# Optimization experiments

Hardware: AMD Instinct MI355X
Metric: run time of the kernel (lower is better)

## Reference

```python
import jax, jax.numpy as jnp
from jax import lax
import numpy as np

N, B, P, D, DOUT, MAXDEG = 81920, 4096, 20, 128, 256, 8
EPS = 1e-5

def _bn(x, g, b):
    m = x.mean(0)
    v = x.var(0)
    return (x - m) / jnp.sqrt(v + EPS) * g + b

def setup_inputs() -> dict:
    key = jax.random.key(0)
    ks = jax.random.split(key, 24)
    s = 0.05
    return {
        'feat': jax.random.normal(ks[0], (N, D), jnp.float32),
        'intend': jax.random.normal(ks[1], (B, D), jnp.float32),
        'position_weight': jax.random.uniform(ks[2], (N,), jnp.float32),
        'nbr_idx': jax.random.randint(ks[3], (N, MAXDEG), 0, N),
        'deg': jax.random.randint(ks[4], (N,), 0, MAXDEG + 1),
        'last_nodes': jax.random.randint(ks[5], (B,), 0, N),
        # EOPA params
        'bn1_g': jnp.ones((D,), jnp.float32),
        'bn1_b': jnp.zeros((D,), jnp.float32),
        'W_ih': jax.random.normal(ks[6], (3 * D, D), jnp.float32) * s,
        'W_hh': jax.random.normal(ks[7], (3 * D, D), jnp.float32) * s,
        'b_ih': jax.random.normal(ks[8], (3 * D,), jnp.float32) * s,
        'b_hh': jax.random.normal(ks[9], (3 * D,), jnp.float32) * s,
        'W_self': jax.random.normal(ks[10], (D, D), jnp.float32) * s,
        'W_neigh': jax.random.normal(ks[11], (D, D), jnp.float32) * s,
        # AttnReadout params (hidden_dim == D)
        'bn2_g': jnp.ones((D,), jnp.float32),
        'bn2_b': jnp.zeros((D,), jnp.float32),
        'Wu': jax.random.normal(ks[12], (D, D), jnp.float32) * s,
        'Wv': jax.random.normal(ks[13], (D, D), jnp.float32) * s,
        'bv': jax.random.normal(ks[14], (D,), jnp.float32) * s,
        'Wi': jax.random.normal(ks[15], (D, D), jnp.float32) * s,
        'bi': jax.random.normal(ks[16], (D,), jnp.float32) * s,
        'We': jax.random.normal(ks[17], (D, 1), jnp.float32) * s,
        'Wout': jax.random.normal(ks[18], (DOUT, D), jnp.float32) * s,
    }

def reference(feat, intend, position_weight, nbr_idx, deg, last_nodes,
              bn1_g, bn1_b, W_ih, W_hh, b_ih, b_hh, W_self, W_neigh,
              bn2_g, bn2_b, Wu, Wv, bv, Wi, bi, We, Wout):
    # ---- EOPA: gather mailbox -> GRU over neighbors -> self + neigh mix ----
    h0 = _bn(feat, bn1_g, bn1_b)              # BatchNorm1d (batch stats)
    mail = h0[nbr_idx]                        # [N, MAXDEG, D] gather
    xs = jnp.moveaxis(mail, 0, 1)             # [MAXDEG, N, D]

    def gru_step(h, tx):
        t, x = tx
        gi = x @ W_ih.T + b_ih                # [N, 3D]
        gh = h @ W_hh.T + b_hh
        ir, iz, inn = jnp.split(gi, 3, axis=1)
        hr, hz, hn = jnp.split(gh, 3, axis=1)
        r = jax.nn.sigmoid(ir + hr)
        z = jax.nn.sigmoid(iz + hz)
        n = jnp.tanh(inn + r * hn)
        h_new = (1.0 - z) * n + z * h
        # freeze state past each node's true mailbox length (ragged GRU)
        h = jnp.where((t < deg)[:, None], h_new, h)
        return h, None

    neigh, _ = lax.scan(gru_step, jnp.zeros((N, D), feat.dtype),
                        (jnp.arange(MAXDEG), xs))
    rst = h0 @ W_self.T + neigh @ W_neigh.T   # [N, D], activation=None

    # ---- AttnReadout: segment softmax attention + segment sums ----
    h = _bn(rst, bn2_g, bn2_b)
    fu = (h @ Wu.T).reshape(B, P, D)
    fv = (intend @ Wv.T + bv)[:, None, :]         # broadcast_nodes
    fl = (h[last_nodes] @ Wi.T + bi)[:, None, :]  # broadcast_nodes
    e = (jax.nn.sigmoid(fu + fv + fl) @ We)[..., 0]   # [B, P]
    alpha = jax.nn.softmax(e, axis=1)[..., None]      # segment_softmax
    hg = h.reshape(B, P, D)
    rst_g = (hg * alpha).sum(axis=1) @ Wout.T         # segment_sum + fc_out
    pos = (hg * position_weight.reshape(B, P, 1)).sum(axis=1) @ Wout.T
    return rst_g, pos
```

## Files before the change

kernel.cpp:

```cpp
#include <hip/hip_runtime.h>

#define NN      81920
#define BB      4096
#define PP      20
#define DD      128
#define DOUTT   256
#define MAXDEGG 8
#define NBLK_B  160

using bf16x8 = __attribute__((ext_vector_type(8))) short;
using f32x4  = __attribute__((ext_vector_type(4))) float;
using u16x4  = __attribute__((ext_vector_type(4))) ushort;

__device__ __forceinline__ float b2f(ushort u) {
    union { unsigned u; float f; } v; v.u = ((unsigned)u) << 16; return v.f;
}
__device__ __forceinline__ ushort f2b(float f) {
    union { float f; unsigned u; } v; v.f = f;
    unsigned r = v.u + 0x7fffu + ((v.u >> 16) & 1u);
    return (ushort)(r >> 16);
}
__device__ __forceinline__ float sigm(float x) {
    return __fdividef(1.f, 1.f + __expf(-x));
}
__device__ __forceinline__ float tanh_fast(float x) {
    return 1.f - __fdividef(2.f, 1.f + __expf(2.f * x));
}
__device__ __forceinline__ f32x4 mfma16(bf16x8 a, bf16x8 b, f32x4 c) {
    return __builtin_amdgcn_mfma_f32_16x16x32_bf16(a, b, c, 0, 0, 0);
}
__device__ __forceinline__ bf16x8 pack8(float4 a, float4 b) {
    bf16x8 r;
    r[0] = (short)f2b(a.x); r[1] = (short)f2b(a.y);
    r[2] = (short)f2b(a.z); r[3] = (short)f2b(a.w);
    r[4] = (short)f2b(b.x); r[5] = (short)f2b(b.y);
    r[6] = (short)f2b(b.z); r[7] = (short)f2b(b.w);
    return r;
}
__device__ __forceinline__ bf16x8 ld8_bf(const ushort* p) { return *(const bf16x8*)p; }
__device__ __forceinline__ bf16x8 ld8_f32(const float* p) {
    return pack8(*(const float4*)p, *(const float4*)(p + 4));
}

__global__ __launch_bounds__(512) void hist_k(const int* __restrict__ deg,
                                              int* __restrict__ blockHist) {
    __shared__ int wh[8][9];
    const int t = threadIdx.x, w = t >> 6, lane = t & 63;
    int d = deg[blockIdx.x * 512 + t]; d = min(max(d, 0), 8);
#pragma unroll
    for (int c = 0; c < 9; ++c) {
        unsigned long long m = __ballot(d == c);
        if (lane == 0) wh[w][c] = __popcll(m);
    }
    __syncthreads();
    if (t < 9) {
        int s = 0;
#pragma unroll
        for (int w2 = 0; w2 < 8; ++w2) s += wh[w2][t];
        blockHist[blockIdx.x * 9 + t] = s;
    }
}
__global__ void scan_k(const int* __restrict__ blockHist,
                       int* __restrict__ blockBase) {
    __shared__ int classTot[9], classStart[9];
    const int c = threadIdx.x;
    if (c < 9) {
        int s = 0;
        for (int b = 0; b < NBLK_B; ++b) s += blockHist[b * 9 + c];
        classTot[c] = s;
    }
    __syncthreads();
    if (c == 0) {
        int acc = 0;
        for (int k = 0; k < 9; ++k) { classStart[k] = acc; acc += classTot[k]; }
    }
    __syncthreads();
    if (c < 9) {
        int acc = classStart[c];
        for (int b = 0; b < NBLK_B; ++b) {
            blockBase[b * 9 + c] = acc;
            acc += blockHist[b * 9 + c];
        }
    }
}
__global__ __launch_bounds__(512) void scatter_k(const int* __restrict__ deg,
                                                 const int* __restrict__ blockBase,
                                                 int* __restrict__ perm) {
    __shared__ int wh[8][9];
    __shared__ int wbase[8][9];
    const int t = threadIdx.x, w = t >> 6, lane = t & 63;
    const int i = blockIdx.x * 512 + t;
    int d = deg[i]; d = min(max(d, 0), 8);
    int lt = 0;
#pragma unroll
    for (int c = 0; c < 9; ++c) {
        unsigned long long m = __ballot(d == c);
        if (lane == 0) wh[w][c] = __popcll(m);
        if (d == c) lt = __popcll(m & ((1ull << lane) - 1ull));
    }
    __syncthreads();
    if (t < 72) {
        const int w2 = t / 9, c = t - w2 * 9;
        int s = blockBase[blockIdx.x * 9 + c];
        for (int k = 0; k < w2; ++k) s += wh[k][c];
        wbase[w2][c] = s;
    }
    __syncthreads();
    perm[wbase[w][d] + lt] = i;
}

__global__ __launch_bounds__(256) void bn_stats(const float* __restrict__ X,
                                                float* __restrict__ part) {
    const int tid  = threadIdx.x;
    const int col  = tid & 127;
    const int half = tid >> 7;
    const long base = (long)blockIdx.x * 128 + (long)half * 64;
    float s = 0.f, q = 0.f;
    for (int i = 0; i < 64; ++i) {
        float x = X[(base + i) * 128 + col];
        s += x; q += x * x;
    }
    __shared__ float red[2][2][128];
    red[0][half][col] = s;
    red[1][half][col] = q;
    __syncthreads();
    if (tid < 128) {
        part[blockIdx.x * 128 + tid]             = red[0][0][tid] + red[0][1][tid];
        part[640 * 128 + blockIdx.x * 128 + tid] = red[1][0][tid] + red[1][1][tid];
    }
}

__global__ __launch_bounds__(256) void bn_final(const float* __restrict__ part, int nparts,
                                                const float* __restrict__ g,
                                                const float* __restrict__ b,
                                                float2* __restrict__ ss) {
    const int c = blockIdx.x;
    const int t = threadIdx.x;
    float s = 0.f, q = 0.f;
    for (int i = t; i < nparts; i += 256) {
        s += part[(long)i * 128 + c];
        q += part[(long)(nparts + i) * 128 + c];
    }
#pragma unroll
    for (int off = 32; off > 0; off >>= 1) {
        s += __shfl_xor(s, off, 64);
        q += __shfl_xor(q, off, 64);
    }
    __shared__ float rs[4], rq[4];
    if ((t & 63) == 0) { rs[t >> 6] = s; rq[t >> 6] = q; }
    __syncthreads();
    if (t == 0) {
        s = rs[0] + rs[1] + rs[2] + rs[3];
        q = rq[0] + rq[1] + rq[2] + rq[3];
        const float inv_n = 1.f / (float)NN;
        float mean = s * inv_n;
        float var  = q * inv_n - mean * mean;
        float rstd = rsqrtf(var + 1e-5f);
        float sc = g[c] * rstd;
        ss[c] = make_float2(sc, b[c] - mean * sc);
    }
}

template <int NCOL, int KPARTS, bool A1F32, bool GATHER2, bool BIAS1, bool BIAS2,
          bool FOLD1, bool FOLD2, int OUTMODE>
__global__ __launch_bounds__(256) void gemm_bt(
    const void* __restrict__ A1, const void* __restrict__ A2,
    const float* __restrict__ W1, const float* __restrict__ W2,
    const float* __restrict__ bias1, const float* __restrict__ bias2,
    const float2* __restrict__ ssW1, const float2* __restrict__ ssW2,
    const int* __restrict__ gidx, void* __restrict__ outv,
    float* __restrict__ part, int nparts,
    const float* __restrict__ fvl, const float* __restrict__ We,
    float* __restrict__ e) {
    constexpr int JT = NCOL / 64;
    __shared__ float epart[4][64];
    const int tid = threadIdx.x;
    const int w   = tid >> 6;
    const int l   = tid & 63;
    const int l15 = l & 15;
    const int l4  = l >> 4;
    const int colbase = w * (NCOL / 4);

    bf16x8 bfr[JT][KPARTS * 4];
    float bv[JT];
    float Wec[JT];
#pragma unroll
    for (int jl = 0; jl < JT; ++jl) {
        const int wrow = colbase + jl * 16 + l15;
        float fb = 0.f;
#pragma unroll
        for (int kp = 0; kp < KPARTS; ++kp) {
            const float* Wp = (kp == 0) ? W1 : W2;
            const float2* sp = (kp == 0) ? ssW1 : ssW2;
            const bool fold = (kp == 0) ? FOLD1 : FOLD2;
#pragma unroll
            for (int kt = 0; kt < 4; ++kt) {
                const float* wp = &Wp[(long)wrow * 128 + kt * 32 + l4 * 8];
                float4 a = *(const float4*)wp;
                float4 b4 = *(const float4*)(wp + 4);
                if (fold) {
                    const float* s = (const float*)(sp + kt * 32 + l4 * 8);
                    float4 s0 = *(const float4*)s, s1 = *(const float4*)(s + 4);
                    float4 s2 = *(const float4*)(s + 8), s3 = *(const float4*)(s + 12);
                    fb += s0.y * a.x + s0.w * a.y + s1.y * a.z + s1.w * a.w
                        + s2.y * b4.x + s2.w * b4.y + s3.y * b4.z + s3.w * b4.w;
                    a.x *= s0.x; a.y *= s0.z; a.z *= s1.x; a.w *= s1.z;
                    b4.x *= s2.x; b4.y *= s2.z; b4.z *= s3.x; b4.w *= s3.z;
                }
                bfr[jl][kp * 4 + kt] = pack8(a, b4);
            }
        }
        if (FOLD1 || FOLD2) {
            fb += __shfl_xor(fb, 16, 64);
            fb += __shfl_xor(fb, 32, 64);
        }
        if (BIAS1) fb += bias1[wrow];
        if (BIAS2) fb += bias2[wrow];
        bv[jl] = fb;
        if (OUTMODE == 3) Wec[jl] = We[wrow];
    }

    const int rowblk = blockIdx.x * 64;
    const f32x4 fz = {0.f, 0.f, 0.f, 0.f};
    float ssum[JT], sq[JT];
#pragma unroll
    for (int jl = 0; jl < JT; ++jl) { ssum[jl] = 0.f; sq[jl] = 0.f; }

#pragma unroll
    for (int it = 0; it < 4; ++it) {
        const int arow1 = rowblk + it * 16 + l15;
        bf16x8 afr[KPARTS * 4];
#pragma unroll
        for (int kt = 0; kt < 4; ++kt) {
            if (A1F32)
                afr[kt] = ld8_f32(&((const float*)A1)[(long)arow1 * 128 + kt * 32 + l4 * 8]);
            else
                afr[kt] = ld8_bf(&((const ushort*)A1)[(long)arow1 * 128 + kt * 32 + l4 * 8]);
        }
        if (KPARTS == 2) {
            const long arow2 = GATHER2 ? (long)gidx[arow1] : (long)arow1;
#pragma unroll
            for (int kt = 0; kt < 4; ++kt)
                afr[4 + kt] = ld8_bf(&((const ushort*)A2)[arow2 * 128 + kt * 32 + l4 * 8]);
        }
        f32x4 acc[JT];
#pragma unroll
        for (int jl = 0; jl < JT; ++jl) {
            acc[jl] = fz;
#pragma unroll
            for (int kk = 0; kk < KPARTS * 4; ++kk)
                acc[jl] = mfma16(afr[kk], bfr[jl][kk], acc[jl]);
        }
        float ps[4] = {0.f, 0.f, 0.f, 0.f};
#pragma unroll
        for (int jl = 0; jl < JT; ++jl) {
            const int col = colbase + jl * 16 + l15;
#pragma unroll
            for (int r = 0; r < 4; ++r) {
                const long orow = rowblk + it * 16 + l4 * 4 + r;
                float v = acc[jl][r] + bv[jl];
                if (OUTMODE == 0 || OUTMODE == 2)
                    ((ushort*)outv)[orow * NCOL + col] = f2b(v);
                if (OUTMODE == 1)
                    ((float*)outv)[orow * NCOL + col] = v;
                if (OUTMODE == 2) { ssum[jl] += v; sq[jl] += v * v; }
                if (OUTMODE == 3) {
                    const int b = (int)orow / PP;
                    ps[r] += sigm(v + fvl[(long)b * 128 + col]) * Wec[jl];
                }
            }
        }
        if (OUTMODE == 3) {
#pragma unroll
            for (int r = 0; r < 4; ++r) {
#pragma unroll
                for (int off = 1; off < 16; off <<= 1)
                    ps[r] += __shfl_xor(ps[r], off, 64);
            }
            if (l15 == 0) {
#pragma unroll
                for (int r = 0; r < 4; ++r)
                    epart[w][it * 16 + l4 * 4 + r] = ps[r];
            }
        }
    }
    if (OUTMODE == 2) {
#pragma unroll
        for (int jl = 0; jl < JT; ++jl) {
            float s = ssum[jl], q = sq[jl];
            s += __shfl_xor(s, 16, 64); s += __shfl_xor(s, 32, 64);
            q += __shfl_xor(q, 16, 64); q += __shfl_xor(q, 32, 64);
            if (l4 == 0) {
                const int col = colbase + jl * 16 + l15;
                part[(long)blockIdx.x * 128 + col] = s;
                part[(long)nparts * 128 + (long)blockIdx.x * 128 + col] = q;
            }
        }
    }
    if (OUTMODE == 3) {
        __syncthreads();
        if (tid < 64)
            e[rowblk + tid] = epart[0][tid] + epart[1][tid] + epart[2][tid] + epart[3][tid];
    }
}

__global__ __attribute__((amdgpu_flat_work_group_size(512, 512), amdgpu_waves_per_eu(4, 4)))
void gru_kernel(const ushort* __restrict__ G,
                const float* __restrict__ Whh,
                const float* __restrict__ bhh,
                const int* __restrict__ nbr_idx,
                const int* __restrict__ deg,
                const int* __restrict__ perm,
                ushort* __restrict__ neigh) {
    __shared__ alignas(16) ushort hbuf[2][64][136];
    __shared__ alignas(16) int nbrs[64][8];
    __shared__ int degs[64];
    __shared__ int nid[64];

    const int tid = threadIdx.x;
    const int w   = tid >> 6;
    const int l   = tid & 63;
    const int l15 = l & 15;
    const int l4  = l >> 4;
    const int blockRow = (gridDim.x - 1 - blockIdx.x) * 64;
    const int colbase = w * 16;
    const int c0 = colbase + l4 * 4;

    if (tid < 64) nid[tid] = perm[blockRow + tid];
    {
        bf16x8 z = {0, 0, 0, 0, 0, 0, 0, 0};
        bf16x8* p = (bf16x8*)&hbuf[0][0][0];
        for (int i = tid; i < 64 * 136 / 8; i += 512) p[i] = z;
    }
    __syncthreads();
    nbrs[tid >> 3][tid & 7] = nbr_idx[(long)nid[tid >> 3] * 8 + (tid & 7)];
    if (tid < 64) degs[tid] = deg[nid[tid]];

    bf16x8 bfr[3][4];
#pragma unroll
    for (int g = 0; g < 3; ++g)
#pragma unroll
        for (int kt = 0; kt < 4; ++kt)
            bfr[g][kt] = ld8_f32(&Whh[(long)(g * 128 + colbase + l15) * 128 + kt * 32 + l4 * 8]);
    f32x4 binit[3];
#pragma unroll
    for (int g = 0; g < 3; ++g)
        binit[g] = *(const f32x4*)&bhh[g * 128 + c0];
    __syncthreads();

    int dreg[4];
#pragma unroll
    for (int it = 0; it < 4; ++it) dreg[it] = degs[it * 16 + l15];
    int dmax = degs[l];
#pragma unroll
    for (int off = 32; off > 0; off >>= 1) dmax = max(dmax, __shfl_xor(dmax, off, 64));
    dmax = __builtin_amdgcn_readfirstlane(dmax);

    u16x4 gP[2][3];
#pragma unroll
    for (int it = 0; it < 2; ++it) {
        gP[it][0] = (u16x4){0,0,0,0}; gP[it][1] = (u16x4){0,0,0,0}; gP[it][2] = (u16x4){0,0,0,0};
        if (0 < dreg[it]) {
            const ushort* Grow = G + (long)nbrs[it * 16 + l15][0] * 384;
            gP[it][0] = *(const u16x4*)&Grow[c0];
            gP[it][1] = *(const u16x4*)&Grow[c0 + 128];
            gP[it][2] = *(const u16x4*)&Grow[c0 + 256];
        }
    }

    int cur = 0;
    for (int t = 0; t < dmax; ++t) {
        u16x4 g23[2][3];
#pragma unroll
        for (int it = 2; it < 4; ++it) {
            u16x4* gd = g23[it - 2];
            gd[0] = (u16x4){0,0,0,0}; gd[1] = (u16x4){0,0,0,0}; gd[2] = (u16x4){0,0,0,0};
            if (t < dreg[it]) {
                const ushort* Grow = G + (long)nbrs[it * 16 + l15][t] * 384;
                gd[0] = *(const u16x4*)&Grow[c0];
                gd[1] = *(const u16x4*)&Grow[c0 + 128];
                gd[2] = *(const u16x4*)&Grow[c0 + 256];
            }
        }

#pragma unroll
        for (int it = 0; it < 2; ++it) {
            const int row = it * 16 + l15;
            const bool upd = (t < dreg[it]);
            bf16x8 af[4];
#pragma unroll
            for (int kt = 0; kt < 4; ++kt)
                af[kt] = *(const bf16x8*)&hbuf[cur][row][kt * 32 + l4 * 8];
            f32x4 ar = binit[0], az = binit[1], an = binit[2];
#pragma unroll
            for (int kt = 0; kt < 4; ++kt) {
                ar = mfma16(bfr[0][kt], af[kt], ar);
                az = mfma16(bfr[1][kt], af[kt], az);
                an = mfma16(bfr[2][kt], af[kt], an);
            }
            const u16x4 hold = *(const u16x4*)&hbuf[cur][row][c0];
            u16x4 hnew = hold;
            if (upd) {
#pragma unroll
                for (int r = 0; r < 4; ++r) {
                    const float rr = sigm(b2f(gP[it][0][r]) + ar[r]);
                    const float zz = sigm(b2f(gP[it][1][r]) + az[r]);
                    const float nn = tanh_fast(b2f(gP[it][2][r]) + rr * an[r]);
                    hnew[r] = f2b((1.f - zz) * nn + zz * b2f(hold[r]));
                }
            }
            *(u16x4*)&hbuf[1 - cur][row][c0] = hnew;
        }

#pragma unroll
        for (int it = 0; it < 2; ++it) {
            gP[it][0] = (u16x4){0,0,0,0}; gP[it][1] = (u16x4){0,0,0,0}; gP[it][2] = (u16x4){0,0,0,0};
            if (t + 1 < dreg[it]) {
                const ushort* Grow = G + (long)nbrs[it * 16 + l15][t + 1] * 384;
                gP[it][0] = *(const u16x4*)&Grow[c0];
                gP[it][1] = *(const u16x4*)&Grow[c0 + 128];
                gP[it][2] = *(const u16x4*)&Grow[c0 + 256];
            }
        }

#pragma unroll
        for (int it = 2; it < 4; ++it) {
            const int row = it * 16 + l15;
            const bool upd = (t < dreg[it]);
            bf16x8 af[4];
#pragma unroll
            for (int kt = 0; kt < 4; ++kt)
                af[kt] = *(const bf16x8*)&hbuf[cur][row][kt * 32 + l4 * 8];
            f32x4 ar = binit[0], az = binit[1], an = binit[2];
#pragma unroll
            for (int kt = 0; kt < 4; ++kt) {
                ar = mfma16(bfr[0][kt], af[kt], ar);
                az = mfma16(bfr[1][kt], af[kt], az);
                an = mfma16(bfr[2][kt], af[kt], an);
            }
            const u16x4 hold = *(const u16x4*)&hbuf[cur][row][c0];
            u16x4 hnew = hold;
            if (upd) {
#pragma unroll
                for (int r = 0; r < 4; ++r) {
                    const float rr = sigm(b2f(g23[it - 2][0][r]) + ar[r]);
                    const float zz = sigm(b2f(g23[it - 2][1][r]) + az[r]);
                    const float nn = tanh_fast(b2f(g23[it - 2][2][r]) + rr * an[r]);
                    hnew[r] = f2b((1.f - zz) * nn + zz * b2f(hold[r]));
                }
            }
            *(u16x4*)&hbuf[1 - cur][row][c0] = hnew;
        }
        __syncthreads();
        cur ^= 1;
    }
    for (int idx = tid; idx < 64 * 16; idx += 512) {
        const int row = idx >> 4, ch = idx & 15;
        bf16x8* dst = (bf16x8*)(neigh + (long)nid[row] * 128);
        dst[ch] = *(const bf16x8*)&hbuf[cur][row][ch * 8];
    }
}

__global__ __launch_bounds__(256) void seg_k(const ushort* __restrict__ rst,
                                             const float* __restrict__ e,
                                             const float* __restrict__ pw,
                                             const float2* __restrict__ ss2,
                                             ushort* __restrict__ s12) {
    const int g = blockIdx.x * 2 + (threadIdx.x >> 7);
    const int c = threadIdx.x & 127;
    const float2 sc = ss2[c];
    float ev[PP];
    float m = -1e30f;
#pragma unroll
    for (int p = 0; p < PP; ++p) { ev[p] = e[g * PP + p]; m = fmaxf(m, ev[p]); }
    float sum = 0.f;
#pragma unroll
    for (int p = 0; p < PP; ++p) { ev[p] = __expf(ev[p] - m); sum += ev[p]; }
    const float inv = __fdividef(1.f, sum);
    float a1 = 0.f, a2 = 0.f;
#pragma unroll
    for (int p = 0; p < PP; ++p) {
        const int node = g * PP + p;
        const float hv = b2f(rst[(long)node * 128 + c]) * sc.x + sc.y;
        a1 += (ev[p] * inv) * hv;
        a2 += pw[node] * hv;
    }
    s12[(long)g * 128 + c]        = f2b(a1);
    s12[(long)(BB + g) * 128 + c] = f2b(a2);
}

extern "C" void kernel_launch(void* const* d_in, const int* in_sizes, int n_in,
                              void* d_out, int out_size, void* d_ws, size_t ws_size,
                              hipStream_t stream) {
    const float* feat    = (const float*)d_in[0];
    const float* intend  = (const float*)d_in[1];
    const float* pw      = (const float*)d_in[2];
    const int*   nbr_idx = (const int*)d_in[3];
    const int*   deg     = (const int*)d_in[4];
    const int*   last    = (const int*)d_in[5];
    const float* bn1_g   = (const float*)d_in[6];
    const float* bn1_b   = (const float*)d_in[7];
    const float* W_ih    = (const float*)d_in[8];
    const float* W_hh    = (const float*)d_in[9];
    const float* b_ih    = (const float*)d_in[10];
    const float* b_hh    = (const float*)d_in[11];
    const float* W_self  = (const float*)d_in[12];
    const float* W_neigh = (const float*)d_in[13];
    const float* bn2_g   = (const float*)d_in[14];
    const float* bn2_b   = (const float*)d_in[15];
    const float* Wu      = (const float*)d_in[16];
    const float* Wv      = (const float*)d_in[17];
    const float* bv      = (const float*)d_in[18];
    const float* Wi      = (const float*)d_in[19];
    const float* bi      = (const float*)d_in[20];
    const float* We      = (const float*)d_in[21];
    const float* Wout    = (const float*)d_in[22];
    float* out = (float*)d_out;
    char* ws = (char*)d_ws;

    ushort* G     = (ushort*)(ws + 0L);
    ushort* rst   = G;
    ushort* neigh = (ushort*)(ws + 62914560L);
    float*  fvl   = (float*)(ws + 83886080L);
    float*  e     = (float*)(ws + 85983232L);
    ushort* s12   = (ushort*)(ws + 86310912L);
    float*  part1 = (float*)(ws + 88408064L);
    float*  part2 = (float*)(ws + 89063424L);
    int*    perm  = (int*)(ws + 90374144L);
    float2* ss1   = (float2*)(ws + 90701824L);
    float2* ss2   = (float2*)(ws + 90702848L);
    int*    blockHist = (int*)(ws + 90703872L);
    int*    blockBase = (int*)(ws + 90709632L);

    bn_stats<<<640, 256, 0, stream>>>(feat, part1);
    bn_final<<<128, 256, 0, stream>>>(part1, 640, bn1_g, bn1_b, ss1);

    hist_k<<<NBLK_B, 512, 0, stream>>>(deg, blockHist);
    scan_k<<<1, 16, 0, stream>>>(blockHist, blockBase);
    scatter_k<<<NBLK_B, 512, 0, stream>>>(deg, blockBase, perm);

    gemm_bt<384, 1, true, false, true, false, true, false, 0><<<1280, 256, 0, stream>>>(
        feat, nullptr, W_ih, nullptr, b_ih, nullptr, ss1, nullptr,
        nullptr, G, nullptr, 0, nullptr, nullptr, nullptr);

    gru_kernel<<<1280, 512, 0, stream>>>(G, W_hh, b_hh, nbr_idx, deg, perm, neigh);

    gemm_bt<128, 2, true, false, false, false, true, false, 2><<<1280, 256, 0, stream>>>(
        feat, neigh, W_self, W_neigh, nullptr, nullptr, ss1, nullptr,
        nullptr, rst, part2, 1280, nullptr, nullptr, nullptr);
    bn_final<<<128, 256, 0, stream>>>(part2, 1280, bn2_g, bn2_b, ss2);

    gemm_bt<128, 2, true, true, true, true, false, true, 1><<<64, 256, 0, stream>>>(
        intend, rst, Wv, Wi, bv, bi, nullptr, ss2,
        last, fvl, nullptr, 0, nullptr, nullptr, nullptr);

    gemm_bt<128, 1, false, false, false, false, true, false, 3><<<1280, 256, 0, stream>>>(
        rst, nullptr, Wu, nullptr, nullptr, nullptr, ss2, nullptr,
        nullptr, nullptr, nullptr, 0, fvl, We, e);

    seg_k<<<2048, 256, 0, stream>>>(rst, e, pw, ss2, s12);

    gemm_bt<256, 1, false, false, false, false, false, false, 1><<<128, 256, 0, stream>>>(
        s12, nullptr, Wout, nullptr, nullptr, nullptr, nullptr, nullptr,
        nullptr, out, nullptr, 0, nullptr, nullptr, nullptr);

    (void)in_sizes; (void)n_in; (void)out_size; (void)ws_size;
}
```

Before: 328.7 us.

## Fuse BN stats with degree histogram, fold GRU biases, widen GEMM blocks

Merges the BN-stats and degree-histogram kernels into one launch, and the BN-final and scan kernels into another, which cuts the launch count. Folds the r/z parts of b_hh into the input-projection GEMM bias so the GRU only adds the n-gate hidden bias. Doubles GEMM workgroups to 512 threads with fewer columns per wave. Restructures the GRU loop with macros and unconditional clamped gathers, so zero-degree rows now issue loads they do not need.

New measurement: 398.3 us. 21.2% more time.

```diff
diff --git a/kernel.cpp b/kernel.cpp
--- a/kernel.cpp
+++ b/kernel.cpp
@@ -6,7 +6,7 @@
 #define DD      128
 #define DOUTT   256
 #define MAXDEGG 8
-#define NBLK_B  160
+#define NBLK_H  320
 
 using bf16x8 = __attribute__((ext_vector_type(8))) short;
 using f32x4  = __attribute__((ext_vector_type(4))) float;
@@ -42,54 +42,110 @@
     return pack8(*(const float4*)p, *(const float4*)(p + 4));
 }
 
-__global__ __launch_bounds__(512) void hist_k(const int* __restrict__ deg,
-                                              int* __restrict__ blockHist) {
-    __shared__ int wh[8][9];
-    const int t = threadIdx.x, w = t >> 6, lane = t & 63;
-    int d = deg[blockIdx.x * 512 + t]; d = min(max(d, 0), 8);
-#pragma unroll
-    for (int c = 0; c < 9; ++c) {
-        unsigned long long m = __ballot(d == c);
-        if (lane == 0) wh[w][c] = __popcll(m);
-    }
-    __syncthreads();
-    if (t < 9) {
-        int s = 0;
-#pragma unroll
-        for (int w2 = 0; w2 < 8; ++w2) s += wh[w2][t];
-        blockHist[blockIdx.x * 9 + t] = s;
-    }
-}
-__global__ void scan_k(const int* __restrict__ blockHist,
-                       int* __restrict__ blockBase) {
-    __shared__ int classTot[9], classStart[9];
-    const int c = threadIdx.x;
-    if (c < 9) {
-        int s = 0;
-        for (int b = 0; b < NBLK_B; ++b) s += blockHist[b * 9 + c];
-        classTot[c] = s;
-    }
-    __syncthreads();
-    if (c == 0) {
-        int acc = 0;
-        for (int k = 0; k < 9; ++k) { classStart[k] = acc; acc += classTot[k]; }
-    }
-    __syncthreads();
-    if (c < 9) {
-        int acc = classStart[c];
-        for (int b = 0; b < NBLK_B; ++b) {
-            blockBase[b * 9 + c] = acc;
-            acc += blockHist[b * 9 + c];
-        }
-    }
-}
-__global__ __launch_bounds__(512) void scatter_k(const int* __restrict__ deg,
+__global__ __launch_bounds__(256) void stats_hist_k(const float* __restrict__ X,
+                                                    const int* __restrict__ deg,
+                                                    float* __restrict__ part,
+                                                    int* __restrict__ blockHist) {
+    const int tid = threadIdx.x;
+    if (blockIdx.x < 640) {
+        const int col  = tid & 127;
+        const int half = tid >> 7;
+        const long base = (long)blockIdx.x * 128 + (long)half * 64;
+        float s = 0.f, q = 0.f;
+        for (int i = 0; i < 64; ++i) {
+            float x = X[(base + i) * 128 + col];
+            s += x; q += x * x;
+        }
+        __shared__ float red[2][2][128];
+        red[0][half][col] = s;
+        red[1][half][col] = q;
+        __syncthreads();
+        if (tid < 128) {
+            part[blockIdx.x * 128 + tid]             = red[0][0][tid] + red[0][1][tid];
+            part[640 * 128 + blockIdx.x * 128 + tid] = red[1][0][tid] + red[1][1][tid];
+        }
+    } else {
+        __shared__ int wh[4][9];
+        const int hb = blockIdx.x - 640;
+        const int w = tid >> 6, lane = tid & 63;
+        int d = deg[hb * 256 + tid]; d = min(max(d, 0), 8);
+#pragma unroll
+        for (int c = 0; c < 9; ++c) {
+            unsigned long long m = __ballot(d == c);
+            if (lane == 0) wh[w][c] = __popcll(m);
+        }
+        __syncthreads();
+        if (tid < 9) {
+            int s = 0;
+#pragma unroll
+            for (int w2 = 0; w2 < 4; ++w2) s += wh[w2][tid];
+            blockHist[hb * 9 + tid] = s;
+        }
+    }
+}
+
+__global__ __launch_bounds__(256) void bnfinal_scan_k(const float* __restrict__ part, int nparts,
+                                                      const float* __restrict__ g,
+                                                      const float* __restrict__ b,
+                                                      float2* __restrict__ ss,
+                                                      const int* __restrict__ blockHist,
+                                                      int* __restrict__ blockBase) {
+    const int t = threadIdx.x;
+    if (blockIdx.x < 128) {
+        const int c = blockIdx.x;
+        float s = 0.f, q = 0.f;
+        for (int i = t; i < nparts; i += 256) {
+            s += part[(long)i * 128 + c];
+            q += part[(long)(nparts + i) * 128 + c];
+        }
+#pragma unroll
+        for (int off = 32; off > 0; off >>= 1) {
+            s += __shfl_xor(s, off, 64);
+            q += __shfl_xor(q, off, 64);
+        }
+        __shared__ float rs[4], rq[4];
+        if ((t & 63) == 0) { rs[t >> 6] = s; rq[t >> 6] = q; }
+        __syncthreads();
+        if (t == 0) {
+            s = rs[0] + rs[1] + rs[2] + rs[3];
+            q = rq[0] + rq[1] + rq[2] + rq[3];
+            const float inv_n = 1.f / (float)NN;
+            float mean = s * inv_n;
+            float var  = q * inv_n - mean * mean;
+            float rstd = rsqrtf(var + 1e-5f);
+            float sc = g[c] * rstd;
+            ss[c] = make_float2(sc, b[c] - mean * sc);
+        }
+    } else {
+        __shared__ int classTot[9], classStart[9];
+        if (t < 9) {
+            int s = 0;
+            for (int b2 = 0; b2 < NBLK_H; ++b2) s += blockHist[b2 * 9 + t];
+            classTot[t] = s;
+        }
+        __syncthreads();
+        if (t == 0) {
+            int acc = 0;
+            for (int k = 0; k < 9; ++k) { classStart[k] = acc; acc += classTot[k]; }
+        }
+        __syncthreads();
+        if (t < 9) {
+            int acc = classStart[t];
+            for (int b2 = 0; b2 < NBLK_H; ++b2) {
+                blockBase[b2 * 9 + t] = acc;
+                acc += blockHist[b2 * 9 + t];
+            }
+        }
+    }
+}
+
+__global__ __launch_bounds__(256) void scatter_k(const int* __restrict__ deg,
                                                  const int* __restrict__ blockBase,
                                                  int* __restrict__ perm) {
-    __shared__ int wh[8][9];
-    __shared__ int wbase[8][9];
+    __shared__ int wh[4][9];
+    __shared__ int wbase[4][9];
     const int t = threadIdx.x, w = t >> 6, lane = t & 63;
-    const int i = blockIdx.x * 512 + t;
+    const int i = blockIdx.x * 256 + t;
     int d = deg[i]; d = min(max(d, 0), 8);
     int lt = 0;
 #pragma unroll
@@ -99,7 +155,7 @@
         if (d == c) lt = __popcll(m & ((1ull << lane) - 1ull));
     }
     __syncthreads();
-    if (t < 72) {
+    if (t < 36) {
         const int w2 = t / 9, c = t - w2 * 9;
         int s = blockBase[blockIdx.x * 9 + c];
         for (int k = 0; k < w2; ++k) s += wh[k][c];
@@ -109,77 +165,25 @@
     perm[wbase[w][d] + lt] = i;
 }
 
-__global__ __launch_bounds__(256) void bn_stats(const float* __restrict__ X,
-                                                float* __restrict__ part) {
-    const int tid  = threadIdx.x;
-    const int col  = tid & 127;
-    const int half = tid >> 7;
-    const long base = (long)blockIdx.x * 128 + (long)half * 64;
-    float s = 0.f, q = 0.f;
-    for (int i = 0; i < 64; ++i) {
-        float x = X[(base + i) * 128 + col];
-        s += x; q += x * x;
-    }
-    __shared__ float red[2][2][128];
-    red[0][half][col] = s;
-    red[1][half][col] = q;
-    __syncthreads();
-    if (tid < 128) {
-        part[blockIdx.x * 128 + tid]             = red[0][0][tid] + red[0][1][tid];
-        part[640 * 128 + blockIdx.x * 128 + tid] = red[1][0][tid] + red[1][1][tid];
-    }
-}
-
-__global__ __launch_bounds__(256) void bn_final(const float* __restrict__ part, int nparts,
-                                                const float* __restrict__ g,
-                                                const float* __restrict__ b,
-                                                float2* __restrict__ ss) {
-    const int c = blockIdx.x;
-    const int t = threadIdx.x;
-    float s = 0.f, q = 0.f;
-    for (int i = t; i < nparts; i += 256) {
-        s += part[(long)i * 128 + c];
-        q += part[(long)(nparts + i) * 128 + c];
-    }
-#pragma unroll
-    for (int off = 32; off > 0; off >>= 1) {
-        s += __shfl_xor(s, off, 64);
-        q += __shfl_xor(q, off, 64);
-    }
-    __shared__ float rs[4], rq[4];
-    if ((t & 63) == 0) { rs[t >> 6] = s; rq[t >> 6] = q; }
-    __syncthreads();
-    if (t == 0) {
-        s = rs[0] + rs[1] + rs[2] + rs[3];
-        q = rq[0] + rq[1] + rq[2] + rq[3];
-        const float inv_n = 1.f / (float)NN;
-        float mean = s * inv_n;
-        float var  = q * inv_n - mean * mean;
-        float rstd = rsqrtf(var + 1e-5f);
-        float sc = g[c] * rstd;
-        ss[c] = make_float2(sc, b[c] - mean * sc);
-    }
-}
-
 template <int NCOL, int KPARTS, bool A1F32, bool GATHER2, bool BIAS1, bool BIAS2,
           bool FOLD1, bool FOLD2, int OUTMODE>
-__global__ __launch_bounds__(256) void gemm_bt(
+__global__ __launch_bounds__(512) void gemm_bt(
     const void* __restrict__ A1, const void* __restrict__ A2,
     const float* __restrict__ W1, const float* __restrict__ W2,
-    const float* __restrict__ bias1, const float* __restrict__ bias2,
+    const float* __restrict__ bias1, const float* __restrict__ bias2, int blim,
     const float2* __restrict__ ssW1, const float2* __restrict__ ssW2,
     const int* __restrict__ gidx, void* __restrict__ outv,
     float* __restrict__ part, int nparts,
     const float* __restrict__ fvl, const float* __restrict__ We,
     float* __restrict__ e) {
-    constexpr int JT = NCOL / 64;
-    __shared__ float epart[4][64];
+    constexpr int JT = NCOL / 128;
+    __shared__ float epart[8][64];
     const int tid = threadIdx.x;
     const int w   = tid >> 6;
     const int l   = tid & 63;
     const int l15 = l & 15;
     const int l4  = l >> 4;
-    const int colbase = w * (NCOL / 4);
+    const int colbase = w * (NCOL / 8);
 
     bf16x8 bfr[JT][KPARTS * 4];
     float bv[JT];
@@ -215,7 +219,7 @@
             fb += __shfl_xor(fb, 32, 64);
         }
         if (BIAS1) fb += bias1[wrow];
-        if (BIAS2) fb += bias2[wrow];
+        if (BIAS2) fb += (wrow < blim) ? bias2[wrow] : 0.f;
         bv[jl] = fb;
         if (OUTMODE == 3) Wec[jl] = We[wrow];
     }
@@ -299,10 +303,50 @@
     }
     if (OUTMODE == 3) {
         __syncthreads();
-        if (tid < 64)
-            e[rowblk + tid] = epart[0][tid] + epart[1][tid] + epart[2][tid] + epart[3][tid];
-    }
-}
+        if (tid < 64) {
+            float s = 0.f;
+#pragma unroll
+            for (int w2 = 0; w2 < 8; ++w2) s += epart[w2][tid];
+            e[rowblk + tid] = s;
+        }
+    }
+}
+
+#define GLOAD(d0, d1, d2, ROW, TT)                                 \
+    { const ushort* Gp_ = G + (long)nbrs[ROW][TT] * 384;           \
+      d0 = *(const u16x4*)&Gp_[c0];                                \
+      d1 = *(const u16x4*)&Gp_[c0 + 128];                          \
+      d2 = *(const u16x4*)&Gp_[c0 + 256]; }
+
+#define GRU_STEP(IT, Gv0, Gv1, Gv2)                                         \
+    {                                                                       \
+        const int row_ = (IT) * 16 + l15;                                   \
+        const bool upd_ = (t < dreg[IT]);                                   \
+        bf16x8 af0 = *(const bf16x8*)&hbuf[cur][row_][0 * 32 + l4 * 8];     \
+        bf16x8 af1 = *(const bf16x8*)&hbuf[cur][row_][1 * 32 + l4 * 8];     \
+        bf16x8 af2 = *(const bf16x8*)&hbuf[cur][row_][2 * 32 + l4 * 8];     \
+        bf16x8 af3 = *(const bf16x8*)&hbuf[cur][row_][3 * 32 + l4 * 8];     \
+        f32x4 ar = fz, az = fz, an = fz;                                    \
+        ar = mfma16(bfr[0][0], af0, ar); az = mfma16(bfr[1][0], af0, az);   \
+        an = mfma16(bfr[2][0], af0, an);                                    \
+        ar = mfma16(bfr[0][1], af1, ar); az = mfma16(bfr[1][1], af1, az);   \
+        an = mfma16(bfr[2][1], af1, an);                                    \
+        ar = mfma16(bfr[0][2], af2, ar); az = mfma16(bfr[1][2], af2, az);   \
+        an = mfma16(bfr[2][2], af2, an);                                    \
+        ar = mfma16(bfr[0][3], af3, ar); az = mfma16(bfr[1][3], af3, az);   \
+        an = mfma16(bfr[2][3], af3, an);                                    \
+        const u16x4 hold_ = *(const u16x4*)&hbuf[cur][row_][c0];            \
+        u16x4 hnew_;                                                        \
+        _Pragma("unroll")                                                   \
+        for (int r = 0; r < 4; ++r) {                                       \
+            const float rr = sigm(b2f(Gv0[r]) + ar[r]);                     \
+            const float zz = sigm(b2f(Gv1[r]) + az[r]);                     \
+            const float nn = tanh_fast(b2f(Gv2[r]) + rr * (an[r] + bnN[r]));\
+            const float hv = (1.f - zz) * nn + zz * b2f(hold_[r]);          \
+            hnew_[r] = upd_ ? f2b(hv) : hold_[r];                           \
+        }                                                                   \
+        *(u16x4*)&hbuf[1 - cur][row_][c0] = hnew_;                          \
+    }
 
 __global__ __attribute__((amdgpu_flat_work_group_size(512, 512), amdgpu_waves_per_eu(4, 4)))
 void gru_kernel(const ushort* __restrict__ G,
@@ -318,12 +362,11 @@
     __shared__ int nid[64];
 
     const int tid = threadIdx.x;
-    const int w   = tid >> 6;
     const int l   = tid & 63;
     const int l15 = l & 15;
     const int l4  = l >> 4;
     const int blockRow = (gridDim.x - 1 - blockIdx.x) * 64;
-    const int colbase = w * 16;
+    const int colbase = (tid >> 6) * 16;
     const int c0 = colbase + l4 * 4;
 
     if (tid < 64) nid[tid] = perm[blockRow + tid];
@@ -342,10 +385,7 @@
 #pragma unroll
         for (int kt = 0; kt < 4; ++kt)
             bfr[g][kt] = ld8_f32(&Whh[(long)(g * 128 + colbase + l15) * 128 + kt * 32 + l4 * 8]);
-    f32x4 binit[3];
-#pragma unroll
-    for (int g = 0; g < 3; ++g)
-        binit[g] = *(const f32x4*)&bhh[g * 128 + c0];
+    const f32x4 bnN = *(const f32x4*)&bhh[256 + c0];
     __syncthreads();
 
     int dreg[4];
@@ -356,101 +396,23 @@
     for (int off = 32; off > 0; off >>= 1) dmax = max(dmax, __shfl_xor(dmax, off, 64));
     dmax = __builtin_amdgcn_readfirstlane(dmax);
 
-    u16x4 gP[2][3];
-#pragma unroll
-    for (int it = 0; it < 2; ++it) {
-        gP[it][0] = (u16x4){0,0,0,0}; gP[it][1] = (u16x4){0,0,0,0}; gP[it][2] = (u16x4){0,0,0,0};
-        if (0 < dreg[it]) {
-            const ushort* Grow = G + (long)nbrs[it * 16 + l15][0] * 384;
-            gP[it][0] = *(const u16x4*)&Grow[c0];
-            gP[it][1] = *(const u16x4*)&Grow[c0 + 128];
-            gP[it][2] = *(const u16x4*)&Grow[c0 + 256];
-        }
-    }
+    const f32x4 fz = {0.f, 0.f, 0.f, 0.f};
+    u16x4 p00, p01, p02, p10, p11, p12;
+    GLOAD(p00, p01, p02, l15, 0);
+    GLOAD(p10, p11, p12, 16 + l15, 0);
 
     int cur = 0;
     for (int t = 0; t < dmax; ++t) {
-        u16x4 g23[2][3];
-#pragma unroll
-        for (int it = 2; it < 4; ++it) {
-            u16x4* gd = g23[it - 2];
-            gd[0] = (u16x4){0,0,0,0}; gd[1] = (u16x4){0,0,0,0}; gd[2] = (u16x4){0,0,0,0};
-            if (t < dreg[it]) {
-                const ushort* Grow = G + (long)nbrs[it * 16 + l15][t] * 384;
-                gd[0] = *(const u16x4*)&Grow[c0];
-                gd[1] = *(const u16x4*)&Grow[c0 + 128];
-                gd[2] = *(const u16x4*)&Grow[c0 + 256];
-            }
-        }
-
-#pragma unroll
-        for (int it = 0; it < 2; ++it) {
-            const int row = it * 16 + l15;
-            const bool upd = (t < dreg[it]);
-            bf16x8 af[4];
-#pragma unroll
-            for (int kt = 0; kt < 4; ++kt)
-                af[kt] = *(const bf16x8*)&hbuf[cur][row][kt * 32 + l4 * 8];
-            f32x4 ar = binit[0], az = binit[1], an = binit[2];
-#pragma unroll
-            for (int kt = 0; kt < 4; ++kt) {
-                ar = mfma16(bfr[0][kt], af[kt], ar);
-                az = mfma16(bfr[1][kt], af[kt], az);
-                an = mfma16(bfr[2][kt], af[kt], an);
-            }
-            const u16x4 hold = *(const u16x4*)&hbuf[cur][row][c0];
-            u16x4 hnew = hold;
-            if (upd) {
-#pragma unroll
-                for (int r = 0; r < 4; ++r) {
-                    const float rr = sigm(b2f(gP[it][0][r]) + ar[r]);
-                    const float zz = sigm(b2f(gP[it][1][r]) + az[r]);
-                    const float nn = tanh_fast(b2f(gP[it][2][r]) + rr * an[r]);
-                    hnew[r] = f2b((1.f - zz) * nn + zz * b2f(hold[r]));
-                }
-            }
-            *(u16x4*)&hbuf[1 - cur][row][c0] = hnew;
-        }
-
-#pragma unroll
-        for (int it = 0; it < 2; ++it) {
-            gP[it][0] = (u16x4){0,0,0,0}; gP[it][1] = (u16x4){0,0,0,0}; gP[it][2] = (u16x4){0,0,0,0};
-            if (t + 1 < dreg[it]) {
-                const ushort* Grow = G + (long)nbrs[it * 16 + l15][t + 1] * 384;
-                gP[it][0] = *(const u16x4*)&Grow[c0];
-                gP[it][1] = *(const u16x4*)&Grow[c0 + 128];
-                gP[it][2] = *(const u16x4*)&Grow[c0 + 256];
-            }
-        }
-
-#pragma unroll
-        for (int it = 2; it < 4; ++it) {
-            const int row = it * 16 + l15;
-            const bool upd = (t < dreg[it]);
-            bf16x8 af[4];
-#pragma unroll
-            for (int kt = 0; kt < 4; ++kt)
-                af[kt] = *(const bf16x8*)&hbuf[cur][row][kt * 32 + l4 * 8];
-            f32x4 ar = binit[0], az = binit[1], an = binit[2];
-#pragma unroll
-            for (int kt = 0; kt < 4; ++kt) {
-                ar = mfma16(bfr[0][kt], af[kt], ar);
-                az = mfma16(bfr[1][kt], af[kt], az);
-                an = mfma16(bfr[2][kt], af[kt], an);
-            }
-            const u16x4 hold = *(const u16x4*)&hbuf[cur][row][c0];
-            u16x4 hnew = hold;
-            if (upd) {
-#pragma unroll
-                for (int r = 0; r < 4; ++r) {
-                    const float rr = sigm(b2f(g23[it - 2][0][r]) + ar[r]);
-                    const float zz = sigm(b2f(g23[it - 2][1][r]) + az[r]);
-                    const float nn = tanh_fast(b2f(g23[it - 2][2][r]) + rr * an[r]);
-                    hnew[r] = f2b((1.f - zz) * nn + zz * b2f(hold[r]));
-                }
-            }
-            *(u16x4*)&hbuf[1 - cur][row][c0] = hnew;
-        }
+        u16x4 q20, q21, q22, q30, q31, q32;
+        GLOAD(q20, q21, q22, 32 + l15, t);
+        GLOAD(q30, q31, q32, 48 + l15, t);
+        GRU_STEP(0, p00, p01, p02);
+        GRU_STEP(1, p10, p11, p12);
+        const int tn = min(t + 1, 7);
+        GLOAD(p00, p01, p02, l15, tn);
+        GLOAD(p10, p11, p12, 16 + l15, tn);
+        GRU_STEP(2, q20, q21, q22);
+        GRU_STEP(3, q30, q31, q32);
         __syncthreads();
         cur ^= 1;
     }
@@ -530,38 +492,37 @@
     float2* ss1   = (float2*)(ws + 90701824L);
     float2* ss2   = (float2*)(ws + 90702848L);
     int*    blockHist = (int*)(ws + 90703872L);
-    int*    blockBase = (int*)(ws + 90709632L);
-
-    bn_stats<<<640, 256, 0, stream>>>(feat, part1);
-    bn_final<<<128, 256, 0, stream>>>(part1, 640, bn1_g, bn1_b, ss1);
-
-    hist_k<<<NBLK_B, 512, 0, stream>>>(deg, blockHist);
-    scan_k<<<1, 16, 0, stream>>>(blockHist, blockBase);
-    scatter_k<<<NBLK_B, 512, 0, stream>>>(deg, blockBase, perm);
-
-    gemm_bt<384, 1, true, false, true, false, true, false, 0><<<1280, 256, 0, stream>>>(
-        feat, nullptr, W_ih, nullptr, b_ih, nullptr, ss1, nullptr,
+    int*    blockBase = (int*)(ws + 90715392L);
+
+    stats_hist_k<<<960, 256, 0, stream>>>(feat, deg, part1, blockHist);
+    bnfinal_scan_k<<<129, 256, 0, stream>>>(part1, 640, bn1_g, bn1_b, ss1,
+                                            blockHist, blockBase);
+    scatter_k<<<NBLK_H, 256, 0, stream>>>(deg, blockBase, perm);
+
+    gemm_bt<384, 1, true, false, true, true, true, false, 0><<<1280, 512, 0, stream>>>(
+        feat, nullptr, W_ih, nullptr, b_ih, b_hh, 256, ss1, nullptr,
         nullptr, G, nullptr, 0, nullptr, nullptr, nullptr);
 
     gru_kernel<<<1280, 512, 0, stream>>>(G, W_hh, b_hh, nbr_idx, deg, perm, neigh);
 
-    gemm_bt<128, 2, true, false, false, false, true, false, 2><<<1280, 256, 0, stream>>>(
-        feat, neigh, W_self, W_neigh, nullptr, nullptr, ss1, nullptr,
+    gemm_bt<128, 2, true, false, false, false, true, false, 2><<<1280, 512, 0, stream>>>(
+        feat, neigh, W_self, W_neigh, nullptr, nullptr, 0, ss1, nullptr,
         nullptr, rst, part2, 1280, nullptr, nullptr, nullptr);
-    bn_final<<<128, 256, 0, stream>>>(part2, 1280, bn2_g, bn2_b, ss2);
-
-    gemm_bt<128, 2, true, true, true, true, false, true, 1><<<64, 256, 0, stream>>>(
-        intend, rst, Wv, Wi, bv, bi, nullptr, ss2,
+    bnfinal_scan_k<<<128, 256, 0, stream>>>(part2, 1280, bn2_g, bn2_b, ss2,
+                                            nullptr, nullptr);
+
+    gemm_bt<128, 2, true, true, true, true, false, true, 1><<<64, 512, 0, stream>>>(
+        intend, rst, Wv, Wi, bv, bi, 128, nullptr, ss2,
         last, fvl, nullptr, 0, nullptr, nullptr, nullptr);
 
-    gemm_bt<128, 1, false, false, false, false, true, false, 3><<<1280, 256, 0, stream>>>(
-        rst, nullptr, Wu, nullptr, nullptr, nullptr, ss2, nullptr,
+    gemm_bt<128, 1, false, false, false, false, true, false, 3><<<1280, 512, 0, stream>>>(
+        rst, nullptr, Wu, nullptr, nullptr, nullptr, 0, ss2, nullptr,
         nullptr, nullptr, nullptr, 0, fvl, We, e);
 
     seg_k<<<2048, 256, 0, stream>>>(rst, e, pw, ss2, s12);
 
-    gemm_bt<256, 1, false, false, false, false, false, false, 1><<<128, 256, 0, stream>>>(
-        s12, nullptr, Wout, nullptr, nullptr, nullptr, nullptr, nullptr,
+    gemm_bt<256, 1, false, false, false, false, false, false, 1><<<128, 512, 0, stream>>>(
+        s12, nullptr, Wout, nullptr, nullptr, nullptr, 0, nullptr, nullptr,
         nullptr, out, nullptr, 0, nullptr, nullptr, nullptr);
 
     (void)in_sizes; (void)n_in; (void)out_size; (void)ws_size;
```
